# Performance work log

Hardware: AMD Instinct MI355X
Metric: run time of the kernel (lower is better)

## Reference

```python
import jax, jax.numpy as jnp
import numpy as np
import math

NUM_SEGMENTS = 4      # num_bezier_segments
SHARPNESS = 75.0
SAMPLE_RATE = 16      # curve samples per bezier segment


def _control_radians(S):
    # replicates the __init__ control-polygon angle construction
    theta = math.pi * 2 / (4 * S) + math.atan(math.tan(2 * math.pi / (4 * S)) / 3.0)
    r = []
    for i in range(S):
        base = 2 * math.pi / S * i
        r += [base, base + theta, 2 * math.pi / S * (i + 1) - theta]
    return jnp.asarray(np.asarray(r, dtype=np.float32).reshape(S, 3))


def _quat_rotate_inv(q, p):
    # rotate p (...,3) by the conjugate of quaternion q (...,4), wxyz convention
    q = q / jnp.linalg.norm(q, axis=-1, keepdims=True)
    w = q[..., 0:1]
    v = -q[..., 1:4]
    t = 2.0 * jnp.cross(v, p)
    return p + w * t + jnp.cross(v, t)


def _csg_stump(points, primitive_parameters, iw, uw, is_training):
    pp = jnp.swapaxes(primitive_parameters, 1, 2)          # (B,K,P)
    B, K, P = pp.shape
    S, R = NUM_SEGMENTS, SAMPLE_RATE
    quat = pp[:, :, :4]
    trans = pp[:, :, 4:7]
    height = pp[:, :, 7]                                   # (B,K)
    radius = jnp.abs(pp[:, :, 8:8 + 3 * S].reshape(B, K, S, 3))
    wts = jnp.abs(pp[:, :, 8 + 3 * S:8 + 5 * S].reshape(B, K, S, 2))

    rad = _control_radians(S)                              # (S,3)
    cp = jnp.stack([jnp.cos(rad) * radius, jnp.sin(rad) * radius], axis=-1)  # (B,K,S,3,2)

    # closed rational cubic bezier spline: segment s uses cp[s,0..2] and cp[s+1,0]
    P0, P1, P2 = cp[:, :, :, 0], cp[:, :, :, 1], cp[:, :, :, 2]
    P3 = jnp.roll(P0, -1, axis=2)
    t = jnp.arange(R, dtype=pp.dtype) / R                  # (R,) endpoint-free
    b0 = (1 - t) ** 3; b1 = 3 * t * (1 - t) ** 2; b2 = 3 * t ** 2 * (1 - t); b3 = t ** 3
    w1 = wts[..., 0:1]; w2 = wts[..., 1:2]                 # (B,K,S,1)
    num = (b0[:, None] * P0[..., None, :]
           + (b1[:, None] * w1[..., None]) * P1[..., None, :]
           + (b2[:, None] * w2[..., None]) * P2[..., None, :]
           + b3[:, None] * P3[..., None, :])               # (B,K,S,R,2)
    den = b0 + b1 * w1 + b2 * w2 + b3                       # (B,K,S,R)
    curve = (num / den[..., None]).reshape(B, K, S * R, 2)  # (B,K,N,2)

    # transform query points into each primitive's local frame
    p_loc = _quat_rotate_inv(quat[:, None], points[:, :, None, :] - trans[:, None])  # (B,M,K,3)
    pxy = p_loc[..., :2]
    pz = p_loc[..., 2]

    # point-to-curve distances without materializing the (B,M,K,N,2) diff
    p_sq = jnp.sum(pxy * pxy, axis=-1)                      # (B,M,K)
    c_sq = jnp.sum(curve * curve, axis=-1)                  # (B,K,N)
    dots = jnp.einsum('bmkd,bknd->bmkn', pxy, curve)
    d = jnp.sqrt(jnp.maximum(p_sq[..., None] + c_sq[:, None] - 2.0 * dots, 0.0) + 1e-12)
    ud = jnp.min(d, axis=-1)                                # (B,M,K) unsigned 2D distance
    idx = jnp.argmin(d, axis=-1)
    curve_r = jnp.sqrt(c_sq)                                # (B,K,N)
    r_near = jnp.take_along_axis(jnp.broadcast_to(curve_r[:, None], d.shape),
                                 idx[..., None], axis=-1)[..., 0]
    sign = jax.lax.stop_gradient(jnp.where(jnp.sqrt(p_sq) <= r_near, -1.0, 1.0))
    sdf2d = sign * ud

    # extrusion along z
    dz = jnp.abs(pz) - height[:, None, :]
    primitive_sdf = (jnp.minimum(jnp.maximum(sdf2d, dz), 0.0)
                     + jnp.sqrt(jnp.maximum(sdf2d, 0.0) ** 2 + jnp.maximum(dz, 0.0) ** 2 + 1e-12))
    support_distances = ud

    occ = jax.nn.sigmoid(-primitive_sdf * SHARPNESS)        # (B,M,K)

    # soft intersection: bkc,bmk->bmkc selection
    pre_i = iw[:, None] * occ[..., None] + (1.0 - iw)[:, None]    # (B,M,K,C)
    if is_training:
        w = jax.lax.stop_gradient(jax.nn.softmax(pre_i * -40.0, axis=-2))
        inter = jnp.sum(w * pre_i, axis=-2)                 # (B,M,C)
    else:
        inter = jnp.min(pre_i, axis=-2)

    # soft union
    pre_u = uw[:, None, :] * inter                          # (B,M,C)
    if is_training:
        w = jax.lax.stop_gradient(jax.nn.softmax(pre_u * 40.0, axis=-1))
        occupancies = jnp.sum(w * pre_u, axis=-1)           # (B,M)
    else:
        occupancies = jnp.max(pre_u, axis=-1)

    return occupancies, primitive_sdf, inter, support_distances


def setup_inputs() -> dict:
    key = jax.random.key(0)
    k1, k2, k3, k4 = jax.random.split(key, 4)
    B, M, K, C = 4, 8192, 64, 32
    P = 8 + 5 * NUM_SEGMENTS  # 28
    return {
        'sample_point_coordinates': jax.random.uniform(k1, (B, M, 3), dtype=jnp.float32),
        'primitive_parameters': jax.random.normal(k2, (B, P, K), dtype=jnp.float32),
        'intersection_layer_weights': jax.random.uniform(k3, (B, K, C), dtype=jnp.float32),
        'union_layer_weights': jax.random.uniform(k4, (B, C), dtype=jnp.float32),
        'is_training': 1,
    }


def reference(sample_point_coordinates, primitive_parameters, intersection_layer_weights,
              union_layer_weights, is_training):
    return _csg_stump(sample_point_coordinates, primitive_parameters,
                      intersection_layer_weights, union_layer_weights, bool(is_training))
```

## Files before the change

kernel.cpp:

```cpp
#include <hip/hip_runtime.h>
#include <math.h>

#define Bb 4
#define Mm 8192
#define Kk 64
#define Cc 32
#define Nn 64
#define Pp 28

#define OFF_PSDF  (Bb*Mm)
#define OFF_INTER (Bb*Mm + Bb*Mm*Kk)
#define OFF_SD    (Bb*Mm + Bb*Mm*Kk + Bb*Mm*Cc)

#define W40    57.707801635558535f
#define NL2_40 (-0.017328679513998632f)
#define S75    108.20212806667225f

typedef float f32x2 __attribute__((ext_vector_type(2)));

struct Rad12 { float v[12]; };

__device__ __forceinline__ float fexp2(float x){ return __builtin_amdgcn_exp2f(x); }
__device__ __forceinline__ float frcp(float x){ return __builtin_amdgcn_rcpf(x); }
__device__ __forceinline__ f32x2 pk_fma(f32x2 a, f32x2 b, f32x2 c){
    f32x2 d;
    asm("v_pk_fma_f32 %0, %1, %2, %3" : "=v"(d) : "v"(a), "v"(b), "v"(c));
    return d;
}

__global__ __launch_bounds__(256)
void curve_prep(const float* __restrict__ pp, Rad12 rad,
                float* __restrict__ ws_cx, float* __restrict__ ws_cy,
                float* __restrict__ ws_cq, float* __restrict__ params_ws)
{
    const int g = blockIdx.x * 256 + threadIdx.x;
    const int k = g & 63;
    const int n = (g >> 6) & 63;
    const int b = g >> 12;

#define PP(p) pp[((b * Pp) + (p)) * Kk + k]

    const int s  = n >> 4;
    const int it = n & 15;
    const float t = (float)it * 0.0625f;
    const int s1 = (s + 1) & 3;

    float r0 = fabsf(PP(8 + 3 * s + 0));
    float r1 = fabsf(PP(8 + 3 * s + 1));
    float r2 = fabsf(PP(8 + 3 * s + 2));
    float r3 = fabsf(PP(8 + 3 * s1 + 0));
    float w1 = fabsf(PP(20 + 2 * s + 0));
    float w2 = fabsf(PP(20 + 2 * s + 1));

    float a0 = rad.v[3 * s + 0], a1 = rad.v[3 * s + 1];
    float a2 = rad.v[3 * s + 2], a3 = rad.v[3 * s1 + 0];

    float P0x = cosf(a0) * r0, P0y = sinf(a0) * r0;
    float P1x = cosf(a1) * r1, P1y = sinf(a1) * r1;
    float P2x = cosf(a2) * r2, P2y = sinf(a2) * r2;
    float P3x = cosf(a3) * r3, P3y = sinf(a3) * r3;

    float omt = 1.0f - t;
    float b0 = omt * omt * omt;
    float b1 = (3.0f * t) * (omt * omt);
    float b2 = (3.0f * (t * t)) * omt;
    float b3 = t * t * t;
    float bw1 = b1 * w1, bw2 = b2 * w2;
    float den = ((b0 + bw1) + bw2) + b3;
    float nx  = ((b0 * P0x + bw1 * P1x) + bw2 * P2x) + b3 * P3x;
    float ny  = ((b0 * P0y + bw1 * P1y) + bw2 * P2y) + b3 * P3y;

    float cx = nx / den, cy = ny / den;
    const int idx = ((b * 32 + (n >> 1)) * 64 + k) * 2 + (n & 1);
    ws_cx[idx] = -2.0f * cx;
    ws_cy[idx] = -2.0f * cy;
    ws_cq[idx] = cx * cx + cy * cy;

    if (n < 8) {
        float val;
        if (n < 4) {
            float q0 = PP(0), q1 = PP(1), q2 = PP(2), q3 = PP(3);
            float nrm = sqrtf(q0 * q0 + q1 * q1 + q2 * q2 + q3 * q3);
            val = PP(n) / nrm;
        } else {
            val = PP(n);
        }
        params_ws[(b * Kk + k) * 8 + n] = val;
    }
#undef PP
}

__global__ __launch_bounds__(1024, 8)
void csg_main(const float* __restrict__ pts, const float* __restrict__ iw_g,
              const float* __restrict__ uw_g, const int* __restrict__ flag,
              const float* __restrict__ ws_cx, const float* __restrict__ ws_cy,
              const float* __restrict__ ws_cq, const float* __restrict__ params_ws,
              float* __restrict__ out)
{
    __shared__ __align__(16) float s_pool[16384];

    const int tid = threadIdx.x;
    const int bid = blockIdx.x;
    const int b   = bid >> 7;
    const int m0  = (bid & 127) << 6;

    {
        ((float4*)&s_pool[0])[tid]     = ((const float4*)(ws_cx + b * 4096))[tid];
        ((float4*)&s_pool[4096])[tid]  = ((const float4*)(ws_cy + b * 4096))[tid];
        ((float4*)&s_pool[8192])[tid]  = ((const float4*)(ws_cq + b * 4096))[tid];
        float w0 = iw_g[b * 2048 + tid];
        float w1 = iw_g[b * 2048 + tid + 1024];
        s_pool[12288 + tid * 2]        = w0 * (-W40);
        s_pool[12288 + tid * 2 + 1]    = (w0 - 1.0f) * W40;
        s_pool[14336 + tid * 2]        = w1 * (-W40);
        s_pool[14336 + tid * 2 + 1]    = (w1 - 1.0f) * W40;
    }
    __syncthreads();

    const int wid  = tid >> 6;
    const int lane = tid & 63;
    const int pt0  = b * Mm + m0 + (wid << 2);

    const int k = lane;
    const float4* prm4 = (const float4*)(params_ws + ((b << 6) + k) * 8);
    float4 q4 = prm4[0];
    float4 t4 = prm4[1];

    const float4* pts4 = (const float4*)(pts + (size_t)pt0 * 3);
    float4 A = pts4[0], Bv = pts4[1], Cv = pts4[2];
    float pxs[4] = {A.x, A.w, Bv.z, Cv.y};
    float pys[4] = {A.y, Bv.x, Bv.w, Cv.z};
    float pzs[4] = {A.z, Bv.y, Cv.x, Cv.w};

    f32x2 plx2[4], ply2[4];
    float plzv[4], psq[4];
    float vx = -q4.y, vy = -q4.z, vz = -q4.w, qw = q4.x;
#pragma unroll
    for (int p = 0; p < 4; ++p) {
        float px = pxs[p] - t4.x, py = pys[p] - t4.y, pz = pzs[p] - t4.z;
        float t1x = 2.0f * (vy * pz - vz * py);
        float t1y = 2.0f * (vz * px - vx * pz);
        float t1z = 2.0f * (vx * py - vy * px);
        float plx = px + qw * t1x + (vy * t1z - vz * t1y);
        float ply = py + qw * t1y + (vz * t1x - vx * t1z);
        plzv[p]   = pz + qw * t1z + (vx * t1y - vy * t1x);
        psq[p]    = plx * plx + ply * ply;
        plx2[p].x = plx; plx2[p].y = plx;
        ply2[p].x = ply; ply2[p].y = ply;
    }

    float best[4] = {1e30f, 1e30f, 1e30f, 1e30f};
    float bcsq[4] = {0.0f, 0.0f, 0.0f, 0.0f};
    const f32x2* cxp = (const f32x2*)&s_pool[k * 2];
    const f32x2* cyp = (const f32x2*)&s_pool[4096 + k * 2];
    const f32x2* cqp = (const f32x2*)&s_pool[8192 + k * 2];
#pragma unroll
    for (int j = 0; j < 32; ++j) {
        f32x2 cx2 = cxp[j * 64];
        f32x2 cy2 = cyp[j * 64];
        f32x2 cq2 = cqp[j * 64];
#pragma unroll
        for (int p = 0; p < 4; ++p) {
            f32x2 d = pk_fma(cx2, plx2[p], pk_fma(cy2, ply2[p], cq2));
            if (d.x < best[p]) { best[p] = d.x; bcsq[p] = cq2.x; }
            if (d.y < best[p]) { best[p] = d.y; bcsq[p] = cq2.y; }
        }
    }

    float occ[4];
#pragma unroll
    for (int p = 0; p < 4; ++p) {
        float d2    = psq[p] + best[p];
        float ud    = sqrtf(fmaxf(d2, 0.0f) + 1e-12f);
        float sgn   = (sqrtf(psq[p]) <= sqrtf(bcsq[p])) ? -1.0f : 1.0f;
        float sdf2d = sgn * ud;
        float dzv   = fabsf(plzv[p]) - t4.w;
        float inner = fminf(fmaxf(sdf2d, dzv), 0.0f);
        float r1m   = fmaxf(sdf2d, 0.0f), r2m = fmaxf(dzv, 0.0f);
        float psdf  = inner + sqrtf(r1m * r1m + r2m * r2m + 1e-12f);
        out[OFF_PSDF + (pt0 + p) * Kk + k] = psdf;
        out[OFF_SD   + (pt0 + p) * Kk + k] = ud;
        occ[p] = frcp(1.0f + fexp2(S75 * psdf));
    }

    __syncthreads();
    *(float4*)&s_pool[8192 + tid * 4] = make_float4(occ[0], occ[1], occ[2], occ[3]);

    const int training = flag[0];
    const int c    = lane & 31;
    const int kb   = lane & 32;
    const float4* occp = (const float4*)&s_pool[8192 + ((wid << 6) + kb) * 4];
    const f32x2*  iwp  = (const f32x2*)&s_pool[12288 + ((kb << 5) + c) * 2];

    float inter[4];
    if (training) {
        float sw[4]  = {0, 0, 0, 0};
        float swp[4] = {0, 0, 0, 0};
#pragma unroll
        for (int j = 0; j < 32; ++j) {
            float4 o4 = occp[j];
            f32x2 wv  = iwp[j * 32];
            float os[4] = {o4.x, o4.y, o4.z, o4.w};
#pragma unroll
            for (int p = 0; p < 4; ++p) {
                float pre = fmaf(wv.x, os[p], wv.y);
                float e   = fexp2(pre);
                sw[p]  += e;
                swp[p]  = fmaf(e, pre, swp[p]);
            }
        }
#pragma unroll
        for (int p = 0; p < 4; ++p) {
            float swt  = sw[p]  + __shfl_xor(sw[p], 32, 64);
            float swpt = swp[p] + __shfl_xor(swp[p], 32, 64);
            inter[p] = swpt * frcp(swt) * NL2_40;
        }
    } else {
        float mx[4] = {-1e30f, -1e30f, -1e30f, -1e30f};
#pragma unroll
        for (int j = 0; j < 32; ++j) {
            float4 o4 = occp[j];
            f32x2 wv  = iwp[j * 32];
            float os[4] = {o4.x, o4.y, o4.z, o4.w};
#pragma unroll
            for (int p = 0; p < 4; ++p)
                mx[p] = fmaxf(mx[p], fmaf(wv.x, os[p], wv.y));
        }
#pragma unroll
        for (int p = 0; p < 4; ++p) {
            float m2 = fmaxf(mx[p], __shfl_xor(mx[p], 32, 64));
            inter[p] = m2 * NL2_40;
        }
    }

    if (lane < Cc) {
#pragma unroll
        for (int p = 0; p < 4; ++p)
            out[OFF_INTER + (pt0 + p) * Cc + c] = inter[p];
    }

    float uwv = uw_g[b * Cc + c];
    float resv[4];
    if (training) {
#pragma unroll
        for (int p = 0; p < 4; ++p) {
            float pu  = uwv * inter[p];
            float e   = fexp2(W40 * pu);
            float num = e * pu, den = e;
#pragma unroll
            for (int msk = 16; msk >= 1; msk >>= 1) {
                num += __shfl_xor(num, msk, 64);
                den += __shfl_xor(den, msk, 64);
            }
            resv[p] = num * frcp(den);
        }
    } else {
#pragma unroll
        for (int p = 0; p < 4; ++p) {
            float pu = uwv * inter[p];
#pragma unroll
            for (int msk = 16; msk >= 1; msk >>= 1)
                pu = fmaxf(pu, __shfl_xor(pu, msk, 64));
            resv[p] = pu;
        }
    }
    if (lane == 0)
        *(float4*)(out + pt0) = make_float4(resv[0], resv[1], resv[2], resv[3]);
}

extern "C" void kernel_launch(void* const* d_in, const int* in_sizes, int n_in,
                              void* d_out, int out_size, void* d_ws, size_t ws_size,
                              hipStream_t stream)
{
    const float* pts  = (const float*)d_in[0];
    const float* pp   = (const float*)d_in[1];
    const float* iw   = (const float*)d_in[2];
    const float* uw   = (const float*)d_in[3];
    const int*   flag = (const int*)d_in[4];
    float* out = (float*)d_out;

    float* ws_cx = (float*)d_ws;
    float* ws_cy = ws_cx + 16384;
    float* ws_cq = ws_cy + 16384;
    float* params_ws = ws_cq + 16384;

    Rad12 rad;
    const double th = M_PI * 2.0 / 16.0 + atan(tan(2.0 * M_PI / 16.0) / 3.0);
    for (int i = 0; i < 4; ++i) {
        double base = 2.0 * M_PI / 4.0 * (double)i;
        rad.v[3 * i + 0] = (float)base;
        rad.v[3 * i + 1] = (float)(base + th);
        rad.v[3 * i + 2] = (float)(2.0 * M_PI / 4.0 * (double)(i + 1) - th);
    }

    curve_prep<<<64, 256, 0, stream>>>(pp, rad, ws_cx, ws_cy, ws_cq, params_ws);
    csg_main<<<Bb * Mm / 64, 1024, 0, stream>>>(pts, iw, uw, flag,
                                                ws_cx, ws_cy, ws_cq, params_ws, out);
}
```

Before: 45.36 us.

## Interleave curve coords in LDS, recompute cq, halve block size, prefetch loops

Curve x and y coordinates are stored interleaved as float4 per k-pair, and the squared norm is recomputed in the inner loop with packed multiply-FMA. This cuts shared memory from 64KB to 48KB and the per-iteration LDS reads to one 128-bit load. Blocks shrink to 512 threads covering 32 points each, giving more blocks per CU. The LDS loads in the distance and intersection loops are software-prefetched one iteration ahead. The cost is extra ALU work per curve sample and more register pressure.

```diff
diff --git a/kernel.cpp b/kernel.cpp
--- a/kernel.cpp
+++ b/kernel.cpp
@@ -17,21 +17,22 @@
 #define S75    108.20212806667225f
 
 typedef float f32x2 __attribute__((ext_vector_type(2)));
+typedef float f32x4 __attribute__((ext_vector_type(4)));
 
 struct Rad12 { float v[12]; };
 
 __device__ __forceinline__ float fexp2(float x){ return __builtin_amdgcn_exp2f(x); }
 __device__ __forceinline__ float frcp(float x){ return __builtin_amdgcn_rcpf(x); }
 __device__ __forceinline__ f32x2 pk_fma(f32x2 a, f32x2 b, f32x2 c){
-    f32x2 d;
-    asm("v_pk_fma_f32 %0, %1, %2, %3" : "=v"(d) : "v"(a), "v"(b), "v"(c));
-    return d;
+    f32x2 d; asm("v_pk_fma_f32 %0, %1, %2, %3" : "=v"(d) : "v"(a), "v"(b), "v"(c)); return d;
+}
+__device__ __forceinline__ f32x2 pk_mul(f32x2 a, f32x2 b){
+    f32x2 d; asm("v_pk_mul_f32 %0, %1, %2" : "=v"(d) : "v"(a), "v"(b)); return d;
 }
 
 __global__ __launch_bounds__(256)
 void curve_prep(const float* __restrict__ pp, Rad12 rad,
-                float* __restrict__ ws_cx, float* __restrict__ ws_cy,
-                float* __restrict__ ws_cq, float* __restrict__ params_ws)
+                float* __restrict__ ws_c, float* __restrict__ params_ws)
 {
     const int g = blockIdx.x * 256 + threadIdx.x;
     const int k = g & 63;
@@ -71,10 +72,10 @@
     float ny  = ((b0 * P0y + bw1 * P1y) + bw2 * P2y) + b3 * P3y;
 
     float cx = nx / den, cy = ny / den;
-    const int idx = ((b * 32 + (n >> 1)) * 64 + k) * 2 + (n & 1);
-    ws_cx[idx] = -2.0f * cx;
-    ws_cy[idx] = -2.0f * cy;
-    ws_cq[idx] = cx * cx + cy * cy;
+    const int j = n >> 1, h = n & 1;
+    float* base = ws_c + (((b * 32 + j) * 64) + k) * 4;
+    base[h]     = -2.0f * cx;
+    base[2 + h] = -2.0f * cy;
 
     if (n < 8) {
         float val;
@@ -90,30 +91,30 @@
 #undef PP
 }
 
-__global__ __launch_bounds__(1024, 8)
+__global__ __launch_bounds__(512, 6)
 void csg_main(const float* __restrict__ pts, const float* __restrict__ iw_g,
               const float* __restrict__ uw_g, const int* __restrict__ flag,
-              const float* __restrict__ ws_cx, const float* __restrict__ ws_cy,
-              const float* __restrict__ ws_cq, const float* __restrict__ params_ws,
+              const float* __restrict__ ws_c, const float* __restrict__ params_ws,
               float* __restrict__ out)
 {
-    __shared__ __align__(16) float s_pool[16384];
+    __shared__ __align__(16) float s_pool[12288];
 
     const int tid = threadIdx.x;
     const int bid = blockIdx.x;
-    const int b   = bid >> 7;
-    const int m0  = (bid & 127) << 6;
+    const int b   = bid >> 8;
+    const int m0  = (bid & 255) << 5;
 
     {
-        ((float4*)&s_pool[0])[tid]     = ((const float4*)(ws_cx + b * 4096))[tid];
-        ((float4*)&s_pool[4096])[tid]  = ((const float4*)(ws_cy + b * 4096))[tid];
-        ((float4*)&s_pool[8192])[tid]  = ((const float4*)(ws_cq + b * 4096))[tid];
-        float w0 = iw_g[b * 2048 + tid];
-        float w1 = iw_g[b * 2048 + tid + 1024];
-        s_pool[12288 + tid * 2]        = w0 * (-W40);
-        s_pool[12288 + tid * 2 + 1]    = (w0 - 1.0f) * W40;
-        s_pool[14336 + tid * 2]        = w1 * (-W40);
-        s_pool[14336 + tid * 2 + 1]    = (w1 - 1.0f) * W40;
+        const f32x4* cs = (const f32x4*)(ws_c + (size_t)b * 8192);
+        f32x4* cd = (f32x4*)s_pool;
+#pragma unroll
+        for (int i = 0; i < 4; ++i) cd[tid + i * 512] = cs[tid + i * 512];
+#pragma unroll
+        for (int i = 0; i < 4; ++i) {
+            float w = iw_g[b * 2048 + tid + i * 512];
+            ((float2*)&s_pool[8192])[tid + i * 512] =
+                make_float2(w * (-W40), (w - 1.0f) * W40);
+        }
     }
     __syncthreads();
 
@@ -132,7 +133,7 @@
     float pys[4] = {A.y, Bv.x, Bv.w, Cv.z};
     float pzs[4] = {A.z, Bv.y, Cv.x, Cv.w};
 
-    f32x2 plx2[4], ply2[4];
+    f32x2 plx4[4], ply4[4];
     float plzv[4], psq[4];
     float vx = -q4.y, vy = -q4.z, vz = -q4.w, qw = q4.x;
 #pragma unroll
@@ -145,34 +146,36 @@
         float ply = py + qw * t1y + (vz * t1x - vx * t1z);
         plzv[p]   = pz + qw * t1z + (vx * t1y - vy * t1x);
         psq[p]    = plx * plx + ply * ply;
-        plx2[p].x = plx; plx2[p].y = plx;
-        ply2[p].x = ply; ply2[p].y = ply;
-    }
-
-    float best[4] = {1e30f, 1e30f, 1e30f, 1e30f};
-    float bcsq[4] = {0.0f, 0.0f, 0.0f, 0.0f};
-    const f32x2* cxp = (const f32x2*)&s_pool[k * 2];
-    const f32x2* cyp = (const f32x2*)&s_pool[4096 + k * 2];
-    const f32x2* cqp = (const f32x2*)&s_pool[8192 + k * 2];
+        float sx = 4.0f * plx, sy = 4.0f * ply;
+        plx4[p].x = sx; plx4[p].y = sx;
+        ply4[p].x = sy; ply4[p].y = sy;
+    }
+
+    float best4[4] = {1e30f, 1e30f, 1e30f, 1e30f};
+    float bcsq4[4] = {0.0f, 0.0f, 0.0f, 0.0f};
+    const f32x4* cbase = ((const f32x4*)s_pool) + k;
+    f32x4 cc = cbase[0];
 #pragma unroll
     for (int j = 0; j < 32; ++j) {
-        f32x2 cx2 = cxp[j * 64];
-        f32x2 cy2 = cyp[j * 64];
-        f32x2 cq2 = cqp[j * 64];
-#pragma unroll
-        for (int p = 0; p < 4; ++p) {
-            f32x2 d = pk_fma(cx2, plx2[p], pk_fma(cy2, ply2[p], cq2));
-            if (d.x < best[p]) { best[p] = d.x; bcsq[p] = cq2.x; }
-            if (d.y < best[p]) { best[p] = d.y; bcsq[p] = cq2.y; }
-        }
+        f32x4 cn = cbase[(((j + 1) & 31)) * 64];
+        f32x2 cx2 = cc.xy, cy2 = cc.zw;
+        f32x2 cq2 = pk_fma(cx2, cx2, pk_mul(cy2, cy2));
+#pragma unroll
+        for (int p = 0; p < 4; ++p) {
+            f32x2 d = pk_fma(cx2, plx4[p], pk_fma(cy2, ply4[p], cq2));
+            if (d.x < best4[p]) { best4[p] = d.x; bcsq4[p] = cq2.x; }
+            if (d.y < best4[p]) { best4[p] = d.y; bcsq4[p] = cq2.y; }
+        }
+        cc = cn;
     }
 
     float occ[4];
 #pragma unroll
     for (int p = 0; p < 4; ++p) {
-        float d2    = psq[p] + best[p];
+        float d2    = psq[p] + 0.25f * best4[p];
+        float bq    = 0.25f * bcsq4[p];
         float ud    = sqrtf(fmaxf(d2, 0.0f) + 1e-12f);
-        float sgn   = (sqrtf(psq[p]) <= sqrtf(bcsq[p])) ? -1.0f : 1.0f;
+        float sgn   = (sqrtf(psq[p]) <= sqrtf(bq)) ? -1.0f : 1.0f;
         float sdf2d = sgn * ud;
         float dzv   = fabsf(plzv[p]) - t4.w;
         float inner = fminf(fmaxf(sdf2d, dzv), 0.0f);
@@ -184,23 +187,29 @@
     }
 
     __syncthreads();
-    *(float4*)&s_pool[8192 + tid * 4] = make_float4(occ[0], occ[1], occ[2], occ[3]);
+    {
+        f32x4 o4; o4.x = occ[0]; o4.y = occ[1]; o4.z = occ[2]; o4.w = occ[3];
+        ((f32x4*)s_pool)[tid] = o4;
+    }
 
     const int training = flag[0];
     const int c    = lane & 31;
     const int kb   = lane & 32;
-    const float4* occp = (const float4*)&s_pool[8192 + ((wid << 6) + kb) * 4];
-    const f32x2*  iwp  = (const f32x2*)&s_pool[12288 + ((kb << 5) + c) * 2];
+    const f32x4* occp = ((const f32x4*)s_pool) + (wid << 6) + kb;
+    const f32x2* iwp  = ((const f32x2*)&s_pool[8192]) + (kb << 5) + c;
 
     float inter[4];
     if (training) {
         float sw[4]  = {0, 0, 0, 0};
         float swp[4] = {0, 0, 0, 0};
+        f32x4 oc = occp[0];
+        f32x2 wv = iwp[0];
 #pragma unroll
         for (int j = 0; j < 32; ++j) {
-            float4 o4 = occp[j];
-            f32x2 wv  = iwp[j * 32];
-            float os[4] = {o4.x, o4.y, o4.z, o4.w};
+            int jn = (j + 1) & 31;
+            f32x4 on = occp[jn];
+            f32x2 wn = iwp[jn * 32];
+            float os[4] = {oc.x, oc.y, oc.z, oc.w};
 #pragma unroll
             for (int p = 0; p < 4; ++p) {
                 float pre = fmaf(wv.x, os[p], wv.y);
@@ -208,6 +217,7 @@
                 sw[p]  += e;
                 swp[p]  = fmaf(e, pre, swp[p]);
             }
+            oc = on; wv = wn;
         }
 #pragma unroll
         for (int p = 0; p < 4; ++p) {
@@ -217,14 +227,18 @@
         }
     } else {
         float mx[4] = {-1e30f, -1e30f, -1e30f, -1e30f};
+        f32x4 oc = occp[0];
+        f32x2 wv = iwp[0];
 #pragma unroll
         for (int j = 0; j < 32; ++j) {
-            float4 o4 = occp[j];
-            f32x2 wv  = iwp[j * 32];
-            float os[4] = {o4.x, o4.y, o4.z, o4.w};
+            int jn = (j + 1) & 31;
+            f32x4 on = occp[jn];
+            f32x2 wn = iwp[jn * 32];
+            float os[4] = {oc.x, oc.y, oc.z, oc.w};
 #pragma unroll
             for (int p = 0; p < 4; ++p)
                 mx[p] = fmaxf(mx[p], fmaf(wv.x, os[p], wv.y));
+            oc = on; wv = wn;
         }
 #pragma unroll
         for (int p = 0; p < 4; ++p) {
@@ -279,10 +293,8 @@
     const int*   flag = (const int*)d_in[4];
     float* out = (float*)d_out;
 
-    float* ws_cx = (float*)d_ws;
-    float* ws_cy = ws_cx + 16384;
-    float* ws_cq = ws_cy + 16384;
-    float* params_ws = ws_cq + 16384;
+    float* ws_c = (float*)d_ws;
+    float* params_ws = ws_c + 32768;
 
     Rad12 rad;
     const double th = M_PI * 2.0 / 16.0 + atan(tan(2.0 * M_PI / 16.0) / 3.0);
@@ -293,7 +305,7 @@
         rad.v[3 * i + 2] = (float)(2.0 * M_PI / 4.0 * (double)(i + 1) - th);
     }
 
-    curve_prep<<<64, 256, 0, stream>>>(pp, rad, ws_cx, ws_cy, ws_cq, params_ws);
-    csg_main<<<Bb * Mm / 64, 1024, 0, stream>>>(pts, iw, uw, flag,
-                                                ws_cx, ws_cy, ws_cq, params_ws, out);
-}
+    curve_prep<<<64, 256, 0, stream>>>(pp, rad, ws_c, params_ws);
+    csg_main<<<Bb * Mm / 32, 512, 0, stream>>>(pts, iw, uw, flag,
+                                               ws_c, params_ws, out);
+}
```

Result: no change. 45.01 us (-0.8%).

## Split main kernel into distance and intersection passes, interleave curve x/y layout

Applied to the files above, without the earlier changes.

Splits the fused kernel into two launches. The first computes the primitive SDFs and writes occupancies to a global workspace. The second loads those occupancies and computes the intersection and union layers in smaller 256-thread blocks. The curve x and y coefficients are interleaved so each inner-loop step does one 16-byte LDS read instead of two 8-byte reads, and the first kernel's shared memory shrinks. In exchange it adds an extra launch and a global round trip of the occupancy tensor (about 8 MB written and read).

```diff
diff --git a/kernel.cpp b/kernel.cpp
--- a/kernel.cpp
+++ b/kernel.cpp
@@ -17,21 +17,20 @@
 #define S75    108.20212806667225f
 
 typedef float f32x2 __attribute__((ext_vector_type(2)));
+typedef float f32x4 __attribute__((ext_vector_type(4)));
 
 struct Rad12 { float v[12]; };
 
 __device__ __forceinline__ float fexp2(float x){ return __builtin_amdgcn_exp2f(x); }
 __device__ __forceinline__ float frcp(float x){ return __builtin_amdgcn_rcpf(x); }
 __device__ __forceinline__ f32x2 pk_fma(f32x2 a, f32x2 b, f32x2 c){
-    f32x2 d;
-    asm("v_pk_fma_f32 %0, %1, %2, %3" : "=v"(d) : "v"(a), "v"(b), "v"(c));
-    return d;
+    f32x2 d; asm("v_pk_fma_f32 %0, %1, %2, %3" : "=v"(d) : "v"(a), "v"(b), "v"(c)); return d;
 }
 
 __global__ __launch_bounds__(256)
 void curve_prep(const float* __restrict__ pp, Rad12 rad,
-                float* __restrict__ ws_cx, float* __restrict__ ws_cy,
-                float* __restrict__ ws_cq, float* __restrict__ params_ws)
+                float* __restrict__ ws_c, float* __restrict__ ws_cq,
+                float* __restrict__ params_ws)
 {
     const int g = blockIdx.x * 256 + threadIdx.x;
     const int k = g & 63;
@@ -71,10 +70,11 @@
     float ny  = ((b0 * P0y + bw1 * P1y) + bw2 * P2y) + b3 * P3y;
 
     float cx = nx / den, cy = ny / den;
-    const int idx = ((b * 32 + (n >> 1)) * 64 + k) * 2 + (n & 1);
-    ws_cx[idx] = -2.0f * cx;
-    ws_cy[idx] = -2.0f * cy;
-    ws_cq[idx] = cx * cx + cy * cy;
+    const int j = n >> 1, h = n & 1;
+    float* base = ws_c + (((b * 32 + j) * 64) + k) * 4;
+    base[h]     = -2.0f * cx;
+    base[2 + h] = -2.0f * cy;
+    ws_cq[(((b * 32 + j) * 64) + k) * 2 + h] = cx * cx + cy * cy;
 
     if (n < 8) {
         float val;
@@ -91,13 +91,13 @@
 }
 
 __global__ __launch_bounds__(1024, 8)
-void csg_main(const float* __restrict__ pts, const float* __restrict__ iw_g,
-              const float* __restrict__ uw_g, const int* __restrict__ flag,
-              const float* __restrict__ ws_cx, const float* __restrict__ ws_cy,
-              const float* __restrict__ ws_cq, const float* __restrict__ params_ws,
-              float* __restrict__ out)
+void csg_p1(const float* __restrict__ pts,
+            const float* __restrict__ ws_c, const float* __restrict__ ws_cq,
+            const float* __restrict__ params_ws,
+            float* __restrict__ occ_ws, float* __restrict__ out)
 {
-    __shared__ __align__(16) float s_pool[16384];
+    __shared__ __align__(16) float s_c[8192];
+    __shared__ __align__(16) float s_q[4096];
 
     const int tid = threadIdx.x;
     const int bid = blockIdx.x;
@@ -105,23 +105,18 @@
     const int m0  = (bid & 127) << 6;
 
     {
-        ((float4*)&s_pool[0])[tid]     = ((const float4*)(ws_cx + b * 4096))[tid];
-        ((float4*)&s_pool[4096])[tid]  = ((const float4*)(ws_cy + b * 4096))[tid];
-        ((float4*)&s_pool[8192])[tid]  = ((const float4*)(ws_cq + b * 4096))[tid];
-        float w0 = iw_g[b * 2048 + tid];
-        float w1 = iw_g[b * 2048 + tid + 1024];
-        s_pool[12288 + tid * 2]        = w0 * (-W40);
-        s_pool[12288 + tid * 2 + 1]    = (w0 - 1.0f) * W40;
-        s_pool[14336 + tid * 2]        = w1 * (-W40);
-        s_pool[14336 + tid * 2 + 1]    = (w1 - 1.0f) * W40;
+        const float4* cs = (const float4*)(ws_c + (size_t)b * 8192);
+        ((float4*)s_c)[tid]        = cs[tid];
+        ((float4*)s_c)[tid + 1024] = cs[tid + 1024];
+        ((float4*)s_q)[tid] = ((const float4*)(ws_cq + (size_t)b * 4096))[tid];
     }
     __syncthreads();
 
     const int wid  = tid >> 6;
     const int lane = tid & 63;
     const int pt0  = b * Mm + m0 + (wid << 2);
-
-    const int k = lane;
+    const int k    = lane;
+
     const float4* prm4 = (const float4*)(params_ws + ((b << 6) + k) * 8);
     float4 q4 = prm4[0];
     float4 t4 = prm4[1];
@@ -151,14 +146,13 @@
 
     float best[4] = {1e30f, 1e30f, 1e30f, 1e30f};
     float bcsq[4] = {0.0f, 0.0f, 0.0f, 0.0f};
-    const f32x2* cxp = (const f32x2*)&s_pool[k * 2];
-    const f32x2* cyp = (const f32x2*)&s_pool[4096 + k * 2];
-    const f32x2* cqp = (const f32x2*)&s_pool[8192 + k * 2];
+    const f32x4* cdp = ((const f32x4*)s_c) + k;
+    const f32x2* cqp = ((const f32x2*)s_q) + k;
 #pragma unroll
     for (int j = 0; j < 32; ++j) {
-        f32x2 cx2 = cxp[j * 64];
-        f32x2 cy2 = cyp[j * 64];
+        f32x4 cd  = cdp[j * 64];
         f32x2 cq2 = cqp[j * 64];
+        f32x2 cx2 = cd.xy, cy2 = cd.zw;
 #pragma unroll
         for (int p = 0; p < 4; ++p) {
             f32x2 d = pk_fma(cx2, plx2[p], pk_fma(cy2, ply2[p], cq2));
@@ -167,7 +161,6 @@
         }
     }
 
-    float occ[4];
 #pragma unroll
     for (int p = 0; p < 4; ++p) {
         float d2    = psq[p] + best[p];
@@ -180,27 +173,66 @@
         float psdf  = inner + sqrtf(r1m * r1m + r2m * r2m + 1e-12f);
         out[OFF_PSDF + (pt0 + p) * Kk + k] = psdf;
         out[OFF_SD   + (pt0 + p) * Kk + k] = ud;
-        occ[p] = frcp(1.0f + fexp2(S75 * psdf));
-    }
-
+        occ_ws[(size_t)(pt0 + p) * Kk + k] = frcp(1.0f + fexp2(S75 * psdf));
+    }
+}
+
+__global__ __launch_bounds__(256, 8)
+void csg_p2(const float* __restrict__ iw_g, const float* __restrict__ uw_g,
+            const int* __restrict__ flag, const float* __restrict__ occ_ws,
+            float* __restrict__ out)
+{
+    __shared__ __align__(16) float2 s_iw[2048];
+    __shared__ __align__(16) float4 s_oq[256];
+
+    const int tid = threadIdx.x;
+    const int bid = blockIdx.x;
+    const int b   = bid >> 9;
+    const int m0  = (bid & 511) << 4;
+    const int pt_base = b * Mm + m0;
+
+#pragma unroll
+    for (int i = 0; i < 8; ++i) {
+        int idx = tid + i * 256;
+        float w = iw_g[b * 2048 + idx];
+        s_iw[idx] = make_float2(w * (-W40), (w - 1.0f) * W40);
+    }
+    {
+        const int pp = tid >> 5, j = tid & 31;
+        const float* oA = occ_ws + (size_t)(pt_base + pp * 2) * Kk;
+        float4 q;
+        q.x = oA[j];       q.y = oA[32 + j];
+        q.z = oA[64 + j];  q.w = oA[96 + j];
+        s_oq[pp * 32 + j] = q;
+    }
     __syncthreads();
-    *(float4*)&s_pool[8192 + tid * 4] = make_float4(occ[0], occ[1], occ[2], occ[3]);
+
+    const int wid  = tid >> 6;
+    const int lane = tid & 63;
+    const int pt0  = pt_base + (wid << 2);
+    const int c    = lane & 31;
+    const bool hi  = lane >= 32;
+    const int kb   = hi ? 32 : 0;
+
+    const float4* oqa = s_oq + (wid << 6);
+    const float4* oqb = oqa + 32;
+    const float2* iwp = s_iw + (kb << 5) + c;
 
     const int training = flag[0];
-    const int c    = lane & 31;
-    const int kb   = lane & 32;
-    const float4* occp = (const float4*)&s_pool[8192 + ((wid << 6) + kb) * 4];
-    const f32x2*  iwp  = (const f32x2*)&s_pool[12288 + ((kb << 5) + c) * 2];
-
     float inter[4];
     if (training) {
         float sw[4]  = {0, 0, 0, 0};
         float swp[4] = {0, 0, 0, 0};
 #pragma unroll
         for (int j = 0; j < 32; ++j) {
-            float4 o4 = occp[j];
-            f32x2 wv  = iwp[j * 32];
-            float os[4] = {o4.x, o4.y, o4.z, o4.w};
+            float4 qa = oqa[j];
+            float4 qb = oqb[j];
+            float2 wv = iwp[j * 32];
+            float os[4];
+            os[0] = hi ? qa.y : qa.x;
+            os[1] = hi ? qa.w : qa.z;
+            os[2] = hi ? qb.y : qb.x;
+            os[3] = hi ? qb.w : qb.z;
 #pragma unroll
             for (int p = 0; p < 4; ++p) {
                 float pre = fmaf(wv.x, os[p], wv.y);
@@ -219,9 +251,14 @@
         float mx[4] = {-1e30f, -1e30f, -1e30f, -1e30f};
 #pragma unroll
         for (int j = 0; j < 32; ++j) {
-            float4 o4 = occp[j];
-            f32x2 wv  = iwp[j * 32];
-            float os[4] = {o4.x, o4.y, o4.z, o4.w};
+            float4 qa = oqa[j];
+            float4 qb = oqb[j];
+            float2 wv = iwp[j * 32];
+            float os[4];
+            os[0] = hi ? qa.y : qa.x;
+            os[1] = hi ? qa.w : qa.z;
+            os[2] = hi ? qb.y : qb.x;
+            os[3] = hi ? qb.w : qb.z;
 #pragma unroll
             for (int p = 0; p < 4; ++p)
                 mx[p] = fmaxf(mx[p], fmaf(wv.x, os[p], wv.y));
@@ -279,10 +316,10 @@
     const int*   flag = (const int*)d_in[4];
     float* out = (float*)d_out;
 
-    float* ws_cx = (float*)d_ws;
-    float* ws_cy = ws_cx + 16384;
-    float* ws_cq = ws_cy + 16384;
-    float* params_ws = ws_cq + 16384;
+    float* ws_c   = (float*)d_ws;
+    float* ws_cq  = ws_c + 32768;
+    float* params = ws_cq + 16384;
+    float* occ_ws = params + 2048;
 
     Rad12 rad;
     const double th = M_PI * 2.0 / 16.0 + atan(tan(2.0 * M_PI / 16.0) / 3.0);
@@ -293,7 +330,8 @@
         rad.v[3 * i + 2] = (float)(2.0 * M_PI / 4.0 * (double)(i + 1) - th);
     }
 
-    curve_prep<<<64, 256, 0, stream>>>(pp, rad, ws_cx, ws_cy, ws_cq, params_ws);
-    csg_main<<<Bb * Mm / 64, 1024, 0, stream>>>(pts, iw, uw, flag,
-                                                ws_cx, ws_cy, ws_cq, params_ws, out);
-}
+    curve_prep<<<64, 256, 0, stream>>>(pp, rad, ws_c, ws_cq, params);
+    csg_p1<<<Bb * Mm / 64, 1024, 0, stream>>>(pts, ws_c, ws_cq, params,
+                                              occ_ws, out);
+    csg_p2<<<Bb * Mm / 16, 256, 0, stream>>>(iw, uw, flag, occ_ws, out);
+}
```

New measurement: 52.39 us. 15.5% more time.
